# Kernel optimization log

Measured on AMD Instinct MI355X. Metric: run time of the kernel, lower is better.

Reference implementation:

```python
import jax, jax.numpy as jnp
import numpy as np

D_MODEL = 1024
N_LAYER = 8
VOCAB = 32000
D_INNER = 2048
D_STATE = 16
DT_RANK = 64  # ceil(d_model/16)
KCONV = 4
SEQ = 2048


def causal_depthwise_conv(u, w):
    # u: [l, d_inner], w: [d_inner, 1, K]; causal padding (K-1, 0), groups=d_inner
    x = u.T[None]  # [1, d_inner, l]
    y = jax.lax.conv_general_dilated(
        x, w, window_strides=(1,), padding=[(KCONV - 1, 0)],
        dimension_numbers=("NCH", "OIH", "NCH"), feature_group_count=u.shape[1])
    return y[0].T  # [l, d_inner]


def selective_scan(u, dt, A, B, C, Dp):
    # u,dt: [l,d_in]; A: [d_in,n]; B,C: [l,n]; D: [d_in]; bilinear discretization
    dt_A = dt[:, :, None] * A[None, :, :]          # [l, d_in, n]
    dt_B = dt[:, :, None] * B[:, None, :]          # [l, d_in, n]
    denom = 1.0 - dt_A / 2
    dA = (1.0 + dt_A / 2) / denom
    dB = dt_B / denom

    def step(h, inp):
        ui, dAi, dBi, Ci = inp
        h = dAi * h + dBi * ui[:, None]            # [d_in, n]
        return h, h @ Ci                           # y_i: [d_in]

    h0 = jnp.zeros((u.shape[1], A.shape[1]), dtype=u.dtype)
    _, y = jax.lax.scan(step, h0, (u, dA, dB, C))
    return y + u * Dp


def mamba_layer(x, Wres, Win, Wconv, WB, WC, Wdt1, Wdt2, bdt, logA, Dp, Wout):
    # RMS pre-norm (no learned scale)
    xn = x * jax.lax.rsqrt(jnp.mean(x * x, axis=-1, keepdims=True) + 1e-6)
    res = xn @ Wres.T                              # [l, d_inner]
    u = xn @ Win.T                                 # [l, d_inner]
    u = causal_depthwise_conv(u, Wconv)
    u = jax.nn.silu(u)
    A = -jnp.exp(logA)                             # [d_inner, n]
    B = u @ WB.T                                   # [l, n]
    C = u @ WC.T                                   # [l, n]
    dt = jax.nn.softplus((u @ Wdt1.T) @ Wdt2.T + bdt)
    y = selective_scan(u, dt, A, B, C, Dp)
    y = y * jax.nn.silu(res)
    return x + y @ Wout.T                          # residual


def setup_inputs() -> dict:
    key = jax.random.key(0)
    ks = jax.random.split(key, 12)
    L = N_LAYER
    token_ids = jax.random.randint(ks[0], (SEQ,), 0, VOCAB)
    embed = jax.random.normal(ks[1], (VOCAB, D_MODEL), jnp.float32) * 0.02
    Wres = jax.random.normal(ks[2], (L, D_INNER, D_MODEL), jnp.float32) * 0.02
    Win = jax.random.normal(ks[3], (L, D_INNER, D_MODEL), jnp.float32) * 0.02
    Wconv = jax.random.normal(ks[4], (L, D_INNER, 1, KCONV), jnp.float32) * 0.3
    WB = jax.random.normal(ks[5], (L, D_STATE, D_INNER), jnp.float32) * 0.02
    WC = jax.random.normal(ks[6], (L, D_STATE, D_INNER), jnp.float32) * 0.02
    Wdt1 = jax.random.normal(ks[7], (L, DT_RANK, D_INNER), jnp.float32) / np.sqrt(D_INNER)
    Wdt2 = jax.random.uniform(ks[8], (L, D_INNER, DT_RANK), jnp.float32,
                              minval=-1 / np.sqrt(DT_RANK), maxval=1 / np.sqrt(DT_RANK))
    # inverse-softplus of dt ~ U[1e-3, 1e-1] in log space
    dt0 = jnp.exp(jax.random.uniform(ks[9], (L, D_INNER)) * (np.log(0.1) - np.log(0.001)) + np.log(0.001))
    bdt = dt0 + jnp.log(-jnp.expm1(-dt0))
    logA = jnp.log(jnp.broadcast_to(jnp.arange(1, D_STATE + 1, dtype=jnp.float32),
                                    (L, D_INNER, D_STATE)))
    Dp = jnp.ones((L, D_INNER), jnp.float32)
    Wout = jax.random.normal(ks[10], (L, D_MODEL, D_INNER), jnp.float32) * 0.02
    return dict(token_ids=token_ids, embed=embed, Wres=Wres, Win=Win, Wconv=Wconv,
                WB=WB, WC=WC, Wdt1=Wdt1, Wdt2=Wdt2, bdt=bdt, logA=logA, Dp=Dp, Wout=Wout)


def reference(token_ids, embed, Wres, Win, Wconv, WB, WC, Wdt1, Wdt2, bdt, logA, Dp, Wout):
    x = embed[token_ids]  # [l, d_model]
    for i in range(Wres.shape[0]):
        x = mamba_layer(x, Wres[i], Win[i], Wconv[i], WB[i], WC[i],
                        Wdt1[i], Wdt2[i], bdt[i], logA[i], Dp[i], Wout[i])
    return x @ embed.T  # [l, vocab] logits (tied embedding)
```

## Files before the change

### kernel.cpp

```cpp
#include <hip/hip_runtime.h>

#define SEQ 2048
#define DMODEL 1024
#define DINNER 2048
#define DSTATE 16
#define DTRANK 64
#define NLAYER 8
#define VOCAB 32000
#define NCHUNK 32
#define CLEN 64
#define PZ 16

typedef float f32x4 __attribute__((ext_vector_type(4)));
typedef short bf16x8 __attribute__((ext_vector_type(8)));

__device__ __forceinline__ ushort f2bf(float f) {
  union { float f; unsigned u; } v; v.f = f;
  unsigned r = v.u + 0x7fffu + ((v.u >> 16) & 1u);
  return (ushort)(r >> 16);
}
__device__ __forceinline__ float bf2f(ushort b) {
  union { unsigned u; float f; } v; v.u = ((unsigned)b) << 16;
  return v.f;
}

__device__ __forceinline__ void lds_load16(const void* g, void* l) {
  __builtin_amdgcn_global_load_lds(
      (const __attribute__((address_space(1))) void*)g,
      (__attribute__((address_space(3))) void*)l, 16, 0, 0);
}

template<int BM, bool NTS>
__global__ __launch_bounds__(512, 2) void gemm8p_bt_bf16(
    const ushort* __restrict__ A, const ushort* __restrict__ B,
    float* __restrict__ C, int N, int K)
{
  constexpr int MFR = BM / 32;
  constexpr int MPP = MFR / 4;
  constexpr int ALOADS = BM / 128;
  __shared__ __align__(16) ushort As[2 * BM * 64];
  __shared__ __align__(16) ushort Bs[2 * 256 * 64];
  const int tid = threadIdx.x;
  const int lane = tid & 63;
  const int wid = tid >> 6;
  const int wr = wid >> 2, wc = wid & 3;
  const int rr = lane & 15, kq = lane >> 4;

  unsigned nwg = gridDim.x * gridDim.y;
  unsigned lb = blockIdx.y * gridDim.x + blockIdx.x;
  if ((nwg & 7u) == 0u) { unsigned cpx = nwg >> 3; lb = (lb & 7u) * cpx + (lb >> 3); }
  const int bm = (int)(lb % gridDim.x) * BM;
  const int bn = (int)(lb / gridDim.x) * 256;

  const ushort* Abase = A + (size_t)bm * K;
  const ushort* Bbase = B + (size_t)bn * K;

  auto stageA = [&](int buf, int h, int kt) {
    constexpr int HR = BM / 2;
#pragma unroll
    for (int L = 0; L < ALOADS; ++L) {
      int f = L * 512 + tid;
      int rl = f >> 3, g = f & 7;
      int gg = g ^ (rl & 7);
      lds_load16(Abase + (size_t)(h * HR + rl) * K + kt * 64 + gg * 8,
                 (void*)(As + buf * (BM * 64) + (h * HR + rl) * 64 + g * 8));
    }
  };
  auto stageB = [&](int buf, int h, int kt) {
#pragma unroll
    for (int L = 0; L < 2; ++L) {
      int f = L * 512 + tid;
      int rl = f >> 3, g = f & 7;
      int gg = g ^ (rl & 7);
      lds_load16(Bbase + (size_t)(h * 128 + rl) * K + kt * 64 + gg * 8,
                 (void*)(Bs + buf * (256 * 64) + (h * 128 + rl) * 64 + g * 8));
    }
  };
  auto rdA = [&](int buf, int r, int kbyte) {
    int sw = kbyte ^ ((r & 7) << 4);
    return *(const bf16x8*)(As + buf * (BM * 64) + r * 64 + (sw >> 1));
  };
  auto rdB = [&](int buf, int r, int kbyte) {
    int sw = kbyte ^ ((r & 7) << 4);
    return *(const bf16x8*)(Bs + buf * (256 * 64) + r * 64 + (sw >> 1));
  };

  f32x4 acc[MFR][4];
#pragma unroll
  for (int m = 0; m < MFR; ++m)
#pragma unroll
    for (int n = 0; n < 4; ++n) acc[m][n] = (f32x4){0.f, 0.f, 0.f, 0.f};

  const int NT = K >> 6;
  stageA(0, 0, 0); stageA(0, 1, 0); stageB(0, 0, 0); stageB(0, 1, 0);

  for (int t = 0; t < NT; ++t) {
    const int cur = t & 1;
    const bool more = (t + 1 < NT);
    if (more) stageA(cur ^ 1, 0, t + 1);
    if (more) {
      if constexpr (BM == 256) asm volatile("s_waitcnt vmcnt(2)" ::: "memory");
      else                     asm volatile("s_waitcnt vmcnt(1)" ::: "memory");
    } else {
      asm volatile("s_waitcnt vmcnt(0)" ::: "memory");
    }
    __syncthreads();

    bf16x8 bfr[4][2];
#pragma unroll
    for (int n = 0; n < 4; ++n)
#pragma unroll
      for (int kk = 0; kk < 2; ++kk)
        bfr[n][kk] = rdB(cur, wc * 64 + n * 16 + rr, kk * 64 + kq * 16);

#pragma unroll
    for (int mq = 0; mq < 4; ++mq) {
      if (mq == 1 && more) stageA(cur ^ 1, 1, t + 1);
      if (mq == 2 && more) stageB(cur ^ 1, 0, t + 1);
      if (mq == 3 && more) stageB(cur ^ 1, 1, t + 1);
      bf16x8 af[MPP][2];
#pragma unroll
      for (int mf = 0; mf < MPP; ++mf)
#pragma unroll
        for (int kk = 0; kk < 2; ++kk)
          af[mf][kk] = rdA(cur, wr * (BM / 2) + (mq * MPP + mf) * 16 + rr, kk * 64 + kq * 16);
      __builtin_amdgcn_s_setprio(1);
#pragma unroll
      for (int kk = 0; kk < 2; ++kk)
#pragma unroll
        for (int mf = 0; mf < MPP; ++mf)
#pragma unroll
          for (int n = 0; n < 4; ++n)
            acc[mq * MPP + mf][n] = __builtin_amdgcn_mfma_f32_16x16x32_bf16(
                af[mf][kk], bfr[n][kk], acc[mq * MPP + mf][n], 0, 0, 0);
      __builtin_amdgcn_s_setprio(0);
    }
    __syncthreads();
  }

  float* ep = (float*)Bs + wid * (16 * 68);
  const int cg = bn + wc * 64;
#pragma unroll
  for (int m = 0; m < MFR; ++m) {
    const int r0g = bm + wr * (BM / 2) + m * 16;
#pragma unroll
    for (int n = 0; n < 4; ++n)
#pragma unroll
      for (int j = 0; j < 4; ++j)
        ep[(kq * 4 + j) * 68 + n * 16 + rr] = acc[m][n][j];
#pragma unroll
    for (int i = 0; i < 4; ++i) {
      int row = i * 4 + kq;
      f32x4 v = *(const f32x4*)&ep[row * 68 + rr * 4];
      f32x4* dst = (f32x4*)&C[(size_t)(r0g + row) * N + cg + rr * 4];
      if constexpr (NTS) __builtin_nontemporal_store(v, dst);
      else *dst = v;
    }
  }
}

template<bool OUTBF>
__global__ __launch_bounds__(256, 2) void gemm2p_bt_bf16(
    const ushort* __restrict__ A, const ushort* __restrict__ B,
    void* __restrict__ Cv, int N, int K)
{
  __shared__ __align__(16) ushort As[2 * 128 * 64];
  __shared__ __align__(16) ushort Bs[2 * 128 * 64];
  const int tid = threadIdx.x;
  const int lane = tid & 63;
  const int wave = tid >> 6;
  const int wr = wave >> 1, wc = wave & 1;
  const int rr = lane & 15, kq = lane >> 4;

  unsigned nwg = gridDim.x * gridDim.y;
  unsigned lb = blockIdx.y * gridDim.x + blockIdx.x;
  if ((nwg & 7u) == 0u) { unsigned cpx = nwg >> 3; lb = (lb & 7u) * cpx + (lb >> 3); }
  const int bm = (int)(lb % gridDim.x) * 128;
  const int bn = (int)(lb / gridDim.x) * 128;

  const ushort* Abase = A + (size_t)bm * K;
  const ushort* Bbase = B + (size_t)bn * K;

  auto stage = [&](int buf, int kt) {
#pragma unroll
    for (int i = 0; i < 4; ++i) {
      int f = i * 256 + tid;
      int rl = f >> 3, g = f & 7;
      int gg = g ^ (rl & 7);
      lds_load16(Abase + (size_t)rl * K + kt * 64 + gg * 8,
                 (void*)(As + buf * 8192 + rl * 64 + g * 8));
      lds_load16(Bbase + (size_t)rl * K + kt * 64 + gg * 8,
                 (void*)(Bs + buf * 8192 + rl * 64 + g * 8));
    }
  };
  auto rdA = [&](int buf, int r, int kbyte) {
    int sw = kbyte ^ ((r & 7) << 4);
    return *(const bf16x8*)(As + buf * 8192 + r * 64 + (sw >> 1));
  };
  auto rdB = [&](int buf, int r, int kbyte) {
    int sw = kbyte ^ ((r & 7) << 4);
    return *(const bf16x8*)(Bs + buf * 8192 + r * 64 + (sw >> 1));
  };

  f32x4 acc[4][4];
#pragma unroll
  for (int m = 0; m < 4; ++m)
#pragma unroll
    for (int n = 0; n < 4; ++n) acc[m][n] = (f32x4){0.f, 0.f, 0.f, 0.f};

  const int NT = K >> 6;
  stage(0, 0);

  for (int t = 0; t < NT; ++t) {
    const int cur = t & 1;
    if (t + 1 < NT) {
      stage(cur ^ 1, t + 1);
      asm volatile("s_waitcnt vmcnt(8)" ::: "memory");
    } else {
      asm volatile("s_waitcnt vmcnt(0)" ::: "memory");
    }
    __syncthreads();
#pragma unroll
    for (int ks = 0; ks < 2; ++ks) {
      const int kbyte = ks * 64 + kq * 16;
      bf16x8 af[4], bfr[4];
#pragma unroll
      for (int m = 0; m < 4; ++m)
        af[m] = rdA(cur, wr * 64 + m * 16 + rr, kbyte);
#pragma unroll
      for (int n = 0; n < 4; ++n)
        bfr[n] = rdB(cur, wc * 64 + n * 16 + rr, kbyte);
      __builtin_amdgcn_s_setprio(1);
#pragma unroll
      for (int m = 0; m < 4; ++m)
#pragma unroll
        for (int n = 0; n < 4; ++n)
          acc[m][n] = __builtin_amdgcn_mfma_f32_16x16x32_bf16(af[m], bfr[n], acc[m][n], 0, 0, 0);
      __builtin_amdgcn_s_setprio(0);
    }
    __syncthreads();
  }

  float* ep = (float*)Bs + wave * (16 * 68);
  const int cg = bn + wc * 64;
#pragma unroll
  for (int m = 0; m < 4; ++m) {
    const int r0g = bm + wr * 64 + m * 16;
#pragma unroll
    for (int n = 0; n < 4; ++n)
#pragma unroll
      for (int j = 0; j < 4; ++j)
        ep[(kq * 4 + j) * 68 + n * 16 + rr] = acc[m][n][j];
#pragma unroll
    for (int i = 0; i < 4; ++i) {
      int row = i * 4 + kq;
      f32x4 v = *(const f32x4*)&ep[row * 68 + rr * 4];
      if constexpr (OUTBF) {
        ushort* C = (ushort*)Cv;
        ushort4 o = {f2bf(v.x), f2bf(v.y), f2bf(v.z), f2bf(v.w)};
        *(ushort4*)&C[(size_t)(r0g + row) * N + cg + rr * 4] = o;
      } else {
        float* C = (float*)Cv;
        *(f32x4*)&C[(size_t)(r0g + row) * N + cg + rr * 4] = v;
      }
    }
  }
}

__global__ __launch_bounds__(256) void gemm_btk_bf16(
    const ushort* __restrict__ A, const ushort* __restrict__ B,
    ushort* __restrict__ Cp, int M, int N, int K)
{
  __shared__ __align__(16) ushort As[128 * 64];
  __shared__ __align__(16) ushort Bs[128 * 64];
  const int tid = threadIdx.x;
  const int lane = tid & 63;
  const int wave = tid >> 6;
  const int wr = wave >> 1, wc = wave & 1;
  const int KC = K / gridDim.z;
  const int k0 = blockIdx.z * KC;

  unsigned nwg = gridDim.x * gridDim.y;
  unsigned lb = blockIdx.y * gridDim.x + blockIdx.x;
  if ((nwg & 7u) == 0u) {
    unsigned cpx = nwg >> 3;
    lb = (lb & 7u) * cpx + (lb >> 3);
  }
  const int bm = (lb % gridDim.x) * 128;
  const int bn = (lb / gridDim.x) * 128;
  const int rr = lane & 15, kq = lane >> 4;

  auto rdA = [&](int r, int kbyte) {
    int sw = kbyte ^ ((r & 7) << 4);
    return *(const bf16x8*)(As + r * 64 + (sw >> 1));
  };
  auto rdB = [&](int r, int kbyte) {
    int sw = kbyte ^ ((r & 7) << 4);
    return *(const bf16x8*)(Bs + r * 64 + (sw >> 1));
  };

  f32x4 acc[4][4];
#pragma unroll
  for (int m = 0; m < 4; ++m)
#pragma unroll
    for (int n = 0; n < 4; ++n) acc[m][n] = (f32x4){0.f, 0.f, 0.f, 0.f};

  for (int kt = 0; kt < KC; kt += 64) {
#pragma unroll
    for (int i = 0; i < 4; ++i) {
      int fb = i * 256 + tid;
      int row = fb >> 3, g = fb & 7;
      int gg = g ^ (row & 7);
      lds_load16(A + (size_t)(bm + row) * K + k0 + kt + gg * 8, (void*)(As + (size_t)fb * 8));
      lds_load16(B + (size_t)(bn + row) * K + k0 + kt + gg * 8, (void*)(Bs + (size_t)fb * 8));
    }
    asm volatile("s_waitcnt vmcnt(0)" ::: "memory");
    __syncthreads();
#pragma unroll
    for (int ks = 0; ks < 2; ++ks) {
      const int kbyte = ks * 64 + kq * 16;
      bf16x8 af[4], bfr[4];
#pragma unroll
      for (int m = 0; m < 4; ++m)
        af[m] = rdA(wr * 64 + m * 16 + rr, kbyte);
#pragma unroll
      for (int n = 0; n < 4; ++n)
        bfr[n] = rdB(wc * 64 + n * 16 + rr, kbyte);
#pragma unroll
      for (int m = 0; m < 4; ++m)
#pragma unroll
        for (int n = 0; n < 4; ++n)
          acc[m][n] = __builtin_amdgcn_mfma_f32_16x16x32_bf16(af[m], bfr[n], acc[m][n], 0, 0, 0);
    }
    __syncthreads();
  }
  ushort* C = Cp + (size_t)blockIdx.z * M * N;
#pragma unroll
  for (int m = 0; m < 4; ++m) {
    const int r0 = bm + wr * 64 + m * 16 + kq * 4;
#pragma unroll
    for (int n = 0; n < 4; ++n) {
      const int cc = bn + wc * 64 + n * 16 + rr;
#pragma unroll
      for (int j = 0; j < 4; ++j)
        C[(size_t)(r0 + j) * N + cc] = f2bf(acc[m][n][j]);
    }
  }
}

__global__ __launch_bounds__(256) void convproj_mfma(
    const ushort* __restrict__ resu0, const ushort* __restrict__ W,
    const float* __restrict__ Wconv, ushort* __restrict__ u,
    float* __restrict__ Cp, int M)
{
  __shared__ __align__(16) ushort u0s[131][128];
  __shared__ __align__(16) ushort As[2][128 * 64];
  __shared__ __align__(16) ushort Bs[2][128 * 64];
  const int tid = threadIdx.x;
  const int lane = tid & 63;
  const int wave = tid >> 6;
  const int wr = wave >> 1, wc = wave & 1;
  const int rr = lane & 15, kq = lane >> 4;
  const int bm = blockIdx.x * 128;
  const int kc = blockIdx.z * 128;

#pragma unroll
  for (int h = 0; h < 2; ++h)
#pragma unroll
    for (int i = 0; i < 4; ++i) {
      int f = i * 256 + tid;
      int rl = f >> 3, g = f & 7;
      int gg = g ^ (rl & 7);
      lds_load16(W + (size_t)rl * DINNER + kc + h * 64 + gg * 8,
                 (void*)(&Bs[h][rl * 64 + g * 8]));
    }

  for (int i = tid; i < 131 * 32; i += 256) {
    int row = i >> 5, c4 = (i & 31) * 4;
    int gr = bm - 3 + row;
    ushort4 v = {0, 0, 0, 0};
    if (gr >= 0)
      v = *(const ushort4*)&resu0[(size_t)gr * (2 * DINNER) + DINNER + kc + c4];
    *(ushort4*)&u0s[row][c4] = v;
  }
  __syncthreads();

  {
    const int c0 = (tid & 31) * 4;
    const int r0 = (tid >> 5) * 16;
    float4 w0 = *(const float4*)&Wconv[(kc + c0 + 0) * 4];
    float4 w1 = *(const float4*)&Wconv[(kc + c0 + 1) * 4];
    float4 w2 = *(const float4*)&Wconv[(kc + c0 + 2) * 4];
    float4 w3 = *(const float4*)&Wconv[(kc + c0 + 3) * 4];
    const int ks = c0 >> 6;
    const int cl = c0 & 63;
    for (int r = r0; r < r0 + 16; ++r) {
      ushort4 a0 = *(const ushort4*)&u0s[r + 0][c0];
      ushort4 a1 = *(const ushort4*)&u0s[r + 1][c0];
      ushort4 a2 = *(const ushort4*)&u0s[r + 2][c0];
      ushort4 a3 = *(const ushort4*)&u0s[r + 3][c0];
      float o0 = bf2f(a0.x) * w0.x + bf2f(a1.x) * w0.y + bf2f(a2.x) * w0.z + bf2f(a3.x) * w0.w;
      float o1 = bf2f(a0.y) * w1.x + bf2f(a1.y) * w1.y + bf2f(a2.y) * w1.z + bf2f(a3.y) * w1.w;
      float o2 = bf2f(a0.z) * w2.x + bf2f(a1.z) * w2.y + bf2f(a2.z) * w2.z + bf2f(a3.z) * w2.w;
      float o3 = bf2f(a0.w) * w3.x + bf2f(a1.w) * w3.y + bf2f(a2.w) * w3.z + bf2f(a3.w) * w3.w;
      o0 = o0 / (1.f + expf(-o0));
      o1 = o1 / (1.f + expf(-o1));
      o2 = o2 / (1.f + expf(-o2));
      o3 = o3 / (1.f + expf(-o3));
      ushort4 o = {f2bf(o0), f2bf(o1), f2bf(o2), f2bf(o3)};
      int sg = ((cl >> 3) ^ (r & 7)) * 8 + (cl & 7);
      *(ushort4*)&As[ks][r * 64 + sg] = o;
      *(ushort4*)&u[(size_t)(bm + r) * DINNER + kc + c0] = o;
    }
  }
  asm volatile("s_waitcnt vmcnt(0)" ::: "memory");
  __syncthreads();

  f32x4 acc[4][4];
#pragma unroll
  for (int m = 0; m < 4; ++m)
#pragma unroll
    for (int n = 0; n < 4; ++n) acc[m][n] = (f32x4){0.f, 0.f, 0.f, 0.f};

#pragma unroll
  for (int ks = 0; ks < 2; ++ks) {
#pragma unroll
    for (int kk = 0; kk < 2; ++kk) {
      const int kbyte = kk * 64 + kq * 16;
      bf16x8 af[4], bfr[4];
#pragma unroll
      for (int m = 0; m < 4; ++m) {
        int r = wr * 64 + m * 16 + rr;
        int sw = kbyte ^ ((r & 7) << 4);
        af[m] = *(const bf16x8*)&As[ks][r * 64 + (sw >> 1)];
      }
#pragma unroll
      for (int n = 0; n < 4; ++n) {
        int r = wc * 64 + n * 16 + rr;
        int sw = kbyte ^ ((r & 7) << 4);
        bfr[n] = *(const bf16x8*)&Bs[ks][r * 64 + (sw >> 1)];
      }
      __builtin_amdgcn_s_setprio(1);
#pragma unroll
      for (int m = 0; m < 4; ++m)
#pragma unroll
        for (int n = 0; n < 4; ++n)
          acc[m][n] = __builtin_amdgcn_mfma_f32_16x16x32_bf16(af[m], bfr[n], acc[m][n], 0, 0, 0);
      __builtin_amdgcn_s_setprio(0);
    }
  }

  float* C = Cp + (size_t)blockIdx.z * M * 128;
#pragma unroll
  for (int m = 0; m < 4; ++m) {
    const int r0 = bm + wr * 64 + m * 16 + kq * 4;
#pragma unroll
    for (int n = 0; n < 4; ++n) {
      const int cc = wc * 64 + n * 16 + rr;
#pragma unroll
      for (int j = 0; j < 4; ++j)
        C[(size_t)(r0 + j) * 128 + cc] = acc[m][n][j];
    }
  }
}

__global__ __launch_bounds__(256) void gemm_dt_bf16(
    const ushort* __restrict__ A, const ushort* __restrict__ W,
    const float* __restrict__ bias, ushort* __restrict__ dt)
{
  __shared__ __align__(16) ushort As[128 * 64];
  __shared__ __align__(16) ushort Bs[128 * 64];
  __shared__ float eps[4 * 16 * 68];
  const int tid = threadIdx.x;
  const int lane = tid & 63;
  const int wave = tid >> 6;
  const int wr = wave >> 1, wc = wave & 1;
  const int rr = lane & 15, kq = lane >> 4;
  const int bm = blockIdx.x * 128;
  const int bn = blockIdx.y * 128;

#pragma unroll
  for (int i = 0; i < 4; ++i) {
    int f = i * 256 + tid;
    int rl = f >> 3, g = f & 7;
    int gg = g ^ (rl & 7);
    lds_load16(A + (size_t)(bm + rl) * DTRANK + gg * 8, (void*)(As + (size_t)f * 8));
    lds_load16(W + (size_t)(bn + rl) * DTRANK + gg * 8, (void*)(Bs + (size_t)f * 8));
  }
  asm volatile("s_waitcnt vmcnt(0)" ::: "memory");
  __syncthreads();

  f32x4 acc[4][4];
#pragma unroll
  for (int m = 0; m < 4; ++m)
#pragma unroll
    for (int n = 0; n < 4; ++n) acc[m][n] = (f32x4){0.f, 0.f, 0.f, 0.f};

#pragma unroll
  for (int ks = 0; ks < 2; ++ks) {
    const int kbyte = ks * 64 + kq * 16;
    bf16x8 af[4], bfr[4];
#pragma unroll
    for (int m = 0; m < 4; ++m) {
      int r = wr * 64 + m * 16 + rr;
      int sw = kbyte ^ ((r & 7) << 4);
      af[m] = *(const bf16x8*)&As[r * 64 + (sw >> 1)];
    }
#pragma unroll
    for (int n = 0; n < 4; ++n) {
      int r = wc * 64 + n * 16 + rr;
      int sw = kbyte ^ ((r & 7) << 4);
      bfr[n] = *(const bf16x8*)&Bs[r * 64 + (sw >> 1)];
    }
#pragma unroll
    for (int m = 0; m < 4; ++m)
#pragma unroll
      for (int n = 0; n < 4; ++n)
        acc[m][n] = __builtin_amdgcn_mfma_f32_16x16x32_bf16(af[m], bfr[n], acc[m][n], 0, 0, 0);
  }
  __syncthreads();

  float* ep = eps + wave * (16 * 68);
  const int cgb = bn + wc * 64 + rr * 4;
  float4 b4 = *(const float4*)&bias[cgb];
#pragma unroll
  for (int m = 0; m < 4; ++m) {
    const int r0g = bm + wr * 64 + m * 16;
#pragma unroll
    for (int n = 0; n < 4; ++n)
#pragma unroll
      for (int j = 0; j < 4; ++j)
        ep[(kq * 4 + j) * 68 + n * 16 + rr] = acc[m][n][j];
#pragma unroll
    for (int i = 0; i < 4; ++i) {
      int row = i * 4 + kq;
      f32x4 v = *(const f32x4*)&ep[row * 68 + rr * 4];
      float v0 = v.x + b4.x, v1 = v.y + b4.y, v2 = v.z + b4.z, v3 = v.w + b4.w;
      v0 = (v0 > 20.f) ? v0 : log1pf(expf(v0));
      v1 = (v1 > 20.f) ? v1 : log1pf(expf(v1));
      v2 = (v2 > 20.f) ? v2 : log1pf(expf(v2));
      v3 = (v3 > 20.f) ? v3 : log1pf(expf(v3));
      ushort4 o = {f2bf(v0), f2bf(v1), f2bf(v2), f2bf(v3)};
      *(ushort4*)&dt[(size_t)(r0g + row) * DINNER + cgb] = o;
    }
  }
}

__global__ __launch_bounds__(256) void add3_rms_kernel(
    const ushort* __restrict__ P0, const ushort* __restrict__ P1,
    float* __restrict__ x, ushort* __restrict__ dst, int donorm)
{
  size_t o = (size_t)blockIdx.x * (DMODEL / 4) + threadIdx.x;
  ushort4 a = ((const ushort4*)P0)[o];
  ushort4 b = ((const ushort4*)P1)[o];
  float4 c = ((float4*)x)[o];
  c.x += bf2f(a.x) + bf2f(b.x);
  c.y += bf2f(a.y) + bf2f(b.y);
  c.z += bf2f(a.z) + bf2f(b.z);
  c.w += bf2f(a.w) + bf2f(b.w);
  ((float4*)x)[o] = c;
  float sc = 1.f;
  if (donorm) {
    float s = c.x * c.x + c.y * c.y + c.z * c.z + c.w * c.w;
#pragma unroll
    for (int off = 32; off > 0; off >>= 1) s += __shfl_down(s, off);
    __shared__ float ws[4];
    if ((threadIdx.x & 63) == 0) ws[threadIdx.x >> 6] = s;
    __syncthreads();
    float tot = ws[0] + ws[1] + ws[2] + ws[3];
    sc = rsqrtf(tot * (1.0f / DMODEL) + 1e-6f);
  }
  ushort4 o4 = {f2bf(c.x * sc), f2bf(c.y * sc), f2bf(c.z * sc), f2bf(c.w * sc)};
  ((ushort4*)dst)[o] = o4;
}

__global__ __launch_bounds__(256) void gather_rms_kernel(
    const int* __restrict__ ids, const float* __restrict__ embed,
    float* __restrict__ x, ushort* __restrict__ xnb)
{
  int row = blockIdx.x;
  int id = ids[row];
  float4 v = ((const float4*)(embed + (size_t)id * DMODEL))[threadIdx.x];
  size_t o = (size_t)row * (DMODEL / 4) + threadIdx.x;
  ((float4*)x)[o] = v;
  float s = v.x * v.x + v.y * v.y + v.z * v.z + v.w * v.w;
#pragma unroll
  for (int off = 32; off > 0; off >>= 1) s += __shfl_down(s, off);
  __shared__ float ws[4];
  if ((threadIdx.x & 63) == 0) ws[threadIdx.x >> 6] = s;
  __syncthreads();
  float tot = ws[0] + ws[1] + ws[2] + ws[3];
  float sc = rsqrtf(tot * (1.0f / DMODEL) + 1e-6f);
  ushort4 o4 = {f2bf(v.x * sc), f2bf(v.y * sc), f2bf(v.z * sc), f2bf(v.w * sc)};
  ((ushort4*)xnb)[o] = o4;
}

__global__ __launch_bounds__(256) void proj_reduce(
    const float* __restrict__ Cp, float* __restrict__ bcdt,
    ushort* __restrict__ dtinb, int M)
{
  int idx = blockIdx.x * 256 + threadIdx.x;
  int row = idx / 96, col = idx - row * 96;
  float s = 0.f;
#pragma unroll
  for (int c = 0; c < PZ; ++c) s += Cp[(size_t)c * M * 128 + (size_t)row * 128 + col];
  if (col < 32) bcdt[(size_t)row * 96 + col] = s;
  else dtinb[(size_t)row * 64 + (col - 32)] = f2bf(s);
}

__global__ __launch_bounds__(256) void scan_pass1(
    const ushort* __restrict__ dt, const ushort* __restrict__ u,
    const float* __restrict__ bcdt, const float* __restrict__ logA,
    float* __restrict__ P, float* __restrict__ S)
{
  const int tid = threadIdx.x;
  const int n = tid & 15, dl = tid >> 4;
  const int dbase = blockIdx.x * 16;
  const int c = blockIdx.y;
  const int t0 = c * CLEN;
  const int d = dbase + dl;
  const float Aval = -expf(logA[d * DSTATE + n]);
  __shared__ float sdt[CLEN][16], su[CLEN][16], sB[CLEN][16];
  {
    int tt = tid >> 2, j0 = (tid & 3) * 4;
    ushort4 rd = *(const ushort4*)&dt[(size_t)(t0 + tt) * DINNER + dbase + j0];
    ushort4 ru = *(const ushort4*)&u[(size_t)(t0 + tt) * DINNER + dbase + j0];
    sdt[tt][j0 + 0] = bf2f(rd.x); sdt[tt][j0 + 1] = bf2f(rd.y);
    sdt[tt][j0 + 2] = bf2f(rd.z); sdt[tt][j0 + 3] = bf2f(rd.w);
    su[tt][j0 + 0] = bf2f(ru.x); su[tt][j0 + 1] = bf2f(ru.y);
    su[tt][j0 + 2] = bf2f(ru.z); su[tt][j0 + 3] = bf2f(ru.w);
    *(float4*)&sB[tt][j0] = *(const float4*)&bcdt[(size_t)(t0 + tt) * 96 + j0];
  }
  __syncthreads();
  float h = 0.f, pr = 1.f;
#pragma unroll 8
  for (int i = 0; i < CLEN; ++i) {
    float dtv = sdt[i][dl], uv = su[i][dl], Bv = sB[i][n];
    float dtA = dtv * Aval;
    float rinv = __builtin_amdgcn_rcpf(1.f - 0.5f * dtA);
    float dA = (1.f + 0.5f * dtA) * rinv;
    float dBu = dtv * Bv * rinv * uv;
    h = dA * h + dBu;
    pr *= dA;
  }
  size_t idx = (size_t)c * (DINNER * DSTATE) + (size_t)d * DSTATE + n;
  P[idx] = pr;
  S[idx] = h;
}

__global__ __launch_bounds__(256) void scan_pass2(
    const ushort* __restrict__ dt, const ushort* __restrict__ u,
    const float* __restrict__ bcdt, const float* __restrict__ logA,
    const float* __restrict__ Dp, const float* __restrict__ P,
    const float* __restrict__ S, const ushort* __restrict__ resu0,
    ushort* __restrict__ y2b)
{
  const int tid = threadIdx.x;
  const int n = tid & 15, dl = tid >> 4;
  const int dbase = blockIdx.x * 16;
  const int c = blockIdx.y;
  const int t0 = c * CLEN;
  const int d = dbase + dl;
  const float Aval = -expf(logA[d * DSTATE + n]);
  const float Dpv = Dp[d];
  __shared__ float sdt[CLEN][16], su[CLEN][16], sB[CLEN][16], sC[CLEN][16], sres[CLEN][16];
  {
    int tt = tid >> 2, j0 = (tid & 3) * 4;
    ushort4 rd = *(const ushort4*)&dt[(size_t)(t0 + tt) * DINNER + dbase + j0];
    ushort4 ru = *(const ushort4*)&u[(size_t)(t0 + tt) * DINNER + dbase + j0];
    ushort4 rr4 = *(const ushort4*)&resu0[(size_t)(t0 + tt) * (2 * DINNER) + dbase + j0];
    sdt[tt][j0 + 0] = bf2f(rd.x); sdt[tt][j0 + 1] = bf2f(rd.y);
    sdt[tt][j0 + 2] = bf2f(rd.z); sdt[tt][j0 + 3] = bf2f(rd.w);
    su[tt][j0 + 0] = bf2f(ru.x); su[tt][j0 + 1] = bf2f(ru.y);
    su[tt][j0 + 2] = bf2f(ru.z); su[tt][j0 + 3] = bf2f(ru.w);
    sres[tt][j0 + 0] = bf2f(rr4.x); sres[tt][j0 + 1] = bf2f(rr4.y);
    sres[tt][j0 + 2] = bf2f(rr4.z); sres[tt][j0 + 3] = bf2f(rr4.w);
    *(float4*)&sB[tt][j0] = *(const float4*)&bcdt[(size_t)(t0 + tt) * 96 + j0];
    *(float4*)&sC[tt][j0] = *(const float4*)&bcdt[(size_t)(t0 + tt) * 96 + 16 + j0];
  }
  float h = 0.f;
  {
    const size_t base = (size_t)d * DSTATE + n;
#pragma unroll 4
    for (int cc = 0; cc < c; ++cc) {
      size_t o = (size_t)cc * (DINNER * DSTATE) + base;
      h = P[o] * h + S[o];
    }
  }
  __syncthreads();
#pragma unroll 4
  for (int i = 0; i < CLEN; ++i) {
    float dtv = sdt[i][dl], uv = su[i][dl];
    float dtA = dtv * Aval;
    float rinv = __builtin_amdgcn_rcpf(1.f - 0.5f * dtA);
    float dA = (1.f + 0.5f * dtA) * rinv;
    float dBu = dtv * sB[i][n] * rinv * uv;
    h = dA * h + dBu;
    float p = h * sC[i][n];
    p += __shfl_xor(p, 1);
    p += __shfl_xor(p, 2);
    p += __shfl_xor(p, 4);
    p += __shfl_xor(p, 8);
    if (n == 0) {
      float rv = sres[i][dl];
      float yv = (p + uv * Dpv) * (rv / (1.f + expf(-rv)));
      y2b[(size_t)(t0 + i) * DINNER + d] = f2bf(yv);
    }
  }
}

__global__ __launch_bounds__(256) void preproc_kernel(
    const float* __restrict__ embed, const float* __restrict__ Wres,
    const float* __restrict__ Win, const float* __restrict__ Wout,
    const float* __restrict__ WB, const float* __restrict__ WC,
    const float* __restrict__ Wdt1, const float* __restrict__ Wdt2,
    ushort* __restrict__ eb, ushort* __restrict__ wcatb,
    ushort* __restrict__ woutb, ushort* __restrict__ wbcdtb,
    ushort* __restrict__ wdt2b)
{
  const size_t S0 = (size_t)VOCAB * DMODEL / 4;
  const size_t S1 = (size_t)NLAYER * 2 * DINNER * DMODEL / 4;
  const size_t S2 = (size_t)NLAYER * DMODEL * DINNER / 4;
  const size_t S3 = (size_t)NLAYER * 128 * DINNER / 4;
  const size_t S4 = (size_t)NLAYER * DINNER * DTRANK / 4;
  size_t i4 = (size_t)blockIdx.x * 256 + threadIdx.x;
  float4 v;
  ushort* dst;
  size_t di;
  if (i4 < S0) {
    v = ((const float4*)embed)[i4];
    dst = eb; di = i4;
  } else if (i4 < S0 + S1) {
    size_t j4 = i4 - S0;
    size_t e0 = j4 * 4;
    int k = (int)(e0 & (DMODEL - 1));
    int r = (int)((e0 >> 10) & (2 * DINNER - 1));
    int l = (int)(e0 >> 22);
    const float* src = (r < DINNER)
        ? &Wres[(((size_t)l * DINNER + r) << 10) + k]
        : &Win[(((size_t)l * DINNER + (r - DINNER)) << 10) + k];
    v = *(const float4*)src;
    dst = wcatb; di = j4;
  } else if (i4 < S0 + S1 + S2) {
    size_t j4 = i4 - S0 - S1;
    v = ((const float4*)Wout)[j4];
    dst = woutb; di = j4;
  } else if (i4 < S0 + S1 + S2 + S3) {
    size_t j4 = i4 - S0 - S1 - S2;
    int k4 = (int)(j4 & (DINNER / 4 - 1));
    int row = (int)((j4 >> 9) & 127);
    int l = (int)(j4 >> 16);
    int k = k4 * 4;
    v = (float4){0.f, 0.f, 0.f, 0.f};
    if (row < 16)       v = *(const float4*)&WB[((size_t)l * DSTATE + row) * DINNER + k];
    else if (row < 32)  v = *(const float4*)&WC[((size_t)l * DSTATE + (row - 16)) * DINNER + k];
    else if (row < 96)  v = *(const float4*)&Wdt1[((size_t)l * DTRANK + (row - 32)) * DINNER + k];
    dst = wbcdtb; di = j4;
  } else if (i4 < S0 + S1 + S2 + S3 + S4) {
    size_t j4 = i4 - S0 - S1 - S2 - S3;
    v = ((const float4*)Wdt2)[j4];
    dst = wdt2b; di = j4;
  } else {
    return;
  }
  ushort4 o = {f2bf(v.x), f2bf(v.y), f2bf(v.z), f2bf(v.w)};
  ((ushort4*)dst)[di] = o;
}

extern "C" void kernel_launch(void* const* d_in, const int* in_sizes, int n_in,
                              void* d_out, int out_size, void* d_ws, size_t ws_size,
                              hipStream_t stream) {
  (void)in_sizes; (void)n_in; (void)out_size;
  const int* token_ids = (const int*)d_in[0];
  const float* embed = (const float*)d_in[1];
  const float* Wres = (const float*)d_in[2];
  const float* Win = (const float*)d_in[3];
  const float* Wconv = (const float*)d_in[4];
  const float* WB = (const float*)d_in[5];
  const float* WC = (const float*)d_in[6];
  const float* Wdt1 = (const float*)d_in[7];
  const float* Wdt2 = (const float*)d_in[8];
  const float* bdt = (const float*)d_in[9];
  const float* logA = (const float*)d_in[10];
  const float* Dp = (const float*)d_in[11];
  const float* Wout = (const float*)d_in[12];
  float* out = (float*)d_out;

  char* w = (char*)d_ws;
  auto alloc = [&](size_t bytes) {
    char* p = w;
    w += (bytes + 255) & ~(size_t)255;
    return p;
  };
  ushort* eb     = (ushort*)alloc((size_t)VOCAB * DMODEL * 2);
  ushort* wcatb  = (ushort*)alloc((size_t)NLAYER * 2 * DINNER * DMODEL * 2);
  ushort* woutb  = (ushort*)alloc((size_t)NLAYER * DMODEL * DINNER * 2);
  ushort* wbcdtb = (ushort*)alloc((size_t)NLAYER * 128 * DINNER * 2);
  ushort* wdt2b  = (ushort*)alloc((size_t)NLAYER * DINNER * DTRANK * 2);
  float* x       = (float*)alloc((size_t)SEQ * DMODEL * 4);
  ushort* xnb    = (ushort*)alloc((size_t)SEQ * DMODEL * 2);
  ushort* resu0  = (ushort*)alloc((size_t)SEQ * 2 * DINNER * 2);
  ushort* u      = (ushort*)alloc((size_t)SEQ * DINNER * 2);
  float* bcdt    = (float*)alloc((size_t)SEQ * 96 * 4);
  ushort* dtinb  = (ushort*)alloc((size_t)SEQ * 64 * 2);
  ushort* dt     = (ushort*)alloc((size_t)SEQ * DINNER * 2);
  float* Cp      = (float*)alloc((size_t)PZ * SEQ * 128 * 4);
  ushort* Cp2    = (ushort*)alloc((size_t)2 * SEQ * DMODEL * 2);
  float* Pbuf    = (float*)alloc((size_t)NCHUNK * DINNER * DSTATE * 4);
  float* Sbuf    = (float*)alloc((size_t)NCHUNK * DINNER * DSTATE * 4);
  ushort* y2b    = (ushort*)alloc((size_t)SEQ * DINNER * 2);
  ushort* xb     = (ushort*)alloc((size_t)SEQ * DMODEL * 2);
  if ((size_t)(w - (char*)d_ws) > ws_size) return;

  {
    size_t total4 = (size_t)VOCAB * DMODEL / 4
                  + (size_t)NLAYER * 2 * DINNER * DMODEL / 4
                  + (size_t)NLAYER * DMODEL * DINNER / 4
                  + (size_t)NLAYER * 128 * DINNER / 4
                  + (size_t)NLAYER * DINNER * DTRANK / 4;
    int nblk = (int)((total4 + 255) / 256);
    preproc_kernel<<<nblk, 256, 0, stream>>>(
        embed, Wres, Win, Wout, WB, WC, Wdt1, Wdt2,
        eb, wcatb, woutb, wbcdtb, wdt2b);
  }
  gather_rms_kernel<<<SEQ, 256, 0, stream>>>(token_ids, embed, x, xnb);

  for (int i = 0; i < NLAYER; ++i) {
    const ushort* wcati = wcatb + (size_t)i * 2 * DINNER * DMODEL;
    const ushort* wouti = woutb + (size_t)i * DMODEL * DINNER;
    const float* wconvi = Wconv + (size_t)i * DINNER * 4;
    const ushort* wbcdtbi = wbcdtb + (size_t)i * 128 * DINNER;
    const ushort* wdt2bi = wdt2b + (size_t)i * DINNER * DTRANK;
    const float* bdti = bdt + (size_t)i * DINNER;
    const float* logAi = logA + (size_t)i * DINNER * DSTATE;
    const float* Dpi = Dp + (size_t)i * DINNER;

    gemm2p_bt_bf16<true><<<dim3(SEQ / 128, 2 * DINNER / 128), 256, 0, stream>>>(
        xnb, wcati, resu0, 2 * DINNER, DMODEL);
    convproj_mfma<<<dim3(SEQ / 128, 1, PZ), 256, 0, stream>>>(
        resu0, wbcdtbi, wconvi, u, Cp, SEQ);
    proj_reduce<<<SEQ * 96 / 256, 256, 0, stream>>>(Cp, bcdt, dtinb, SEQ);
    gemm_dt_bf16<<<dim3(SEQ / 128, DINNER / 128), 256, 0, stream>>>(
        dtinb, wdt2bi, bdti, dt);
    dim3 gs(DINNER / 16, NCHUNK);
    scan_pass1<<<gs, 256, 0, stream>>>(dt, u, bcdt, logAi, Pbuf, Sbuf);
    scan_pass2<<<gs, 256, 0, stream>>>(dt, u, bcdt, logAi, Dpi, Pbuf, Sbuf, resu0, y2b);
    gemm_btk_bf16<<<dim3(SEQ / 128, DMODEL / 128, 2), 256, 0, stream>>>(
        y2b, wouti, Cp2, SEQ, DMODEL, DINNER);
    add3_rms_kernel<<<SEQ, 256, 0, stream>>>(
        Cp2, Cp2 + (size_t)SEQ * DMODEL, x,
        (i < NLAYER - 1) ? xnb : xb, (i < NLAYER - 1) ? 1 : 0);
  }
  gemm8p_bt_bf16<256, true><<<dim3(SEQ / 256, VOCAB / 256), 512, 0, stream>>>(
      xb, eb, out, VOCAB, DMODEL);
}
```

Baseline: 1.910 ms.

## Fuse dt projection GEMM and softplus into both scan passes

Measured after the change: 1.986 ms. +4.0%, slower.

```diff
diff --git a/kernel.cpp b/kernel.cpp
--- a/kernel.cpp
+++ b/kernel.cpp
@@ -464,88 +464,6 @@
   }
 }
 
-__global__ __launch_bounds__(256) void gemm_dt_bf16(
-    const ushort* __restrict__ A, const ushort* __restrict__ W,
-    const float* __restrict__ bias, ushort* __restrict__ dt)
-{
-  __shared__ __align__(16) ushort As[128 * 64];
-  __shared__ __align__(16) ushort Bs[128 * 64];
-  __shared__ float eps[4 * 16 * 68];
-  const int tid = threadIdx.x;
-  const int lane = tid & 63;
-  const int wave = tid >> 6;
-  const int wr = wave >> 1, wc = wave & 1;
-  const int rr = lane & 15, kq = lane >> 4;
-  const int bm = blockIdx.x * 128;
-  const int bn = blockIdx.y * 128;
-
-#pragma unroll
-  for (int i = 0; i < 4; ++i) {
-    int f = i * 256 + tid;
-    int rl = f >> 3, g = f & 7;
-    int gg = g ^ (rl & 7);
-    lds_load16(A + (size_t)(bm + rl) * DTRANK + gg * 8, (void*)(As + (size_t)f * 8));
-    lds_load16(W + (size_t)(bn + rl) * DTRANK + gg * 8, (void*)(Bs + (size_t)f * 8));
-  }
-  asm volatile("s_waitcnt vmcnt(0)" ::: "memory");
-  __syncthreads();
-
-  f32x4 acc[4][4];
-#pragma unroll
-  for (int m = 0; m < 4; ++m)
-#pragma unroll
-    for (int n = 0; n < 4; ++n) acc[m][n] = (f32x4){0.f, 0.f, 0.f, 0.f};
-
-#pragma unroll
-  for (int ks = 0; ks < 2; ++ks) {
-    const int kbyte = ks * 64 + kq * 16;
-    bf16x8 af[4], bfr[4];
-#pragma unroll
-    for (int m = 0; m < 4; ++m) {
-      int r = wr * 64 + m * 16 + rr;
-      int sw = kbyte ^ ((r & 7) << 4);
-      af[m] = *(const bf16x8*)&As[r * 64 + (sw >> 1)];
-    }
-#pragma unroll
-    for (int n = 0; n < 4; ++n) {
-      int r = wc * 64 + n * 16 + rr;
-      int sw = kbyte ^ ((r & 7) << 4);
-      bfr[n] = *(const bf16x8*)&Bs[r * 64 + (sw >> 1)];
-    }
-#pragma unroll
-    for (int m = 0; m < 4; ++m)
-#pragma unroll
-      for (int n = 0; n < 4; ++n)
-        acc[m][n] = __builtin_amdgcn_mfma_f32_16x16x32_bf16(af[m], bfr[n], acc[m][n], 0, 0, 0);
-  }
-  __syncthreads();
-
-  float* ep = eps + wave * (16 * 68);
-  const int cgb = bn + wc * 64 + rr * 4;
-  float4 b4 = *(const float4*)&bias[cgb];
-#pragma unroll
-  for (int m = 0; m < 4; ++m) {
-    const int r0g = bm + wr * 64 + m * 16;
-#pragma unroll
-    for (int n = 0; n < 4; ++n)
-#pragma unroll
-      for (int j = 0; j < 4; ++j)
-        ep[(kq * 4 + j) * 68 + n * 16 + rr] = acc[m][n][j];
-#pragma unroll
-    for (int i = 0; i < 4; ++i) {
-      int row = i * 4 + kq;
-      f32x4 v = *(const f32x4*)&ep[row * 68 + rr * 4];
-      float v0 = v.x + b4.x, v1 = v.y + b4.y, v2 = v.z + b4.z, v3 = v.w + b4.w;
-      v0 = (v0 > 20.f) ? v0 : log1pf(expf(v0));
-      v1 = (v1 > 20.f) ? v1 : log1pf(expf(v1));
-      v2 = (v2 > 20.f) ? v2 : log1pf(expf(v2));
-      v3 = (v3 > 20.f) ? v3 : log1pf(expf(v3));
-      ushort4 o = {f2bf(v0), f2bf(v1), f2bf(v2), f2bf(v3)};
-      *(ushort4*)&dt[(size_t)(r0g + row) * DINNER + cgb] = o;
-    }
-  }
-}
-
 __global__ __launch_bounds__(256) void add3_rms_kernel(
     const ushort* __restrict__ P0, const ushort* __restrict__ P1,
     float* __restrict__ x, ushort* __restrict__ dst, int donorm)
@@ -608,9 +526,35 @@
   else dtinb[(size_t)row * 64 + (col - 32)] = f2bf(s);
 }
 
+__device__ __forceinline__ void compute_dt_tile(
+    const ushort* sDtin , const ushort* sW2 ,
+    const float* __restrict__ bdt, int dbase,
+    float sdt[CLEN][16], int tid)
+{
+  const int wave = tid >> 6;
+  const int lane = tid & 63;
+  f32x4 dacc = (f32x4){0.f, 0.f, 0.f, 0.f};
+#pragma unroll
+  for (int ks = 0; ks < 2; ++ks) {
+    bf16x8 af = *(const bf16x8*)&sDtin[(wave * 16 + (lane & 15)) * 64 + ks * 32 + (lane >> 4) * 8];
+    bf16x8 bf = *(const bf16x8*)&sW2[(lane & 15) * 64 + ks * 32 + (lane >> 4) * 8];
+    dacc = __builtin_amdgcn_mfma_f32_16x16x32_bf16(af, bf, dacc, 0, 0, 0);
+  }
+  const int col = lane & 15;
+  const float bv = bdt[dbase + col];
+#pragma unroll
+  for (int j = 0; j < 4; ++j) {
+    int trow = wave * 16 + (lane >> 4) * 4 + j;
+    float v = dacc[j] + bv;
+    v = (v > 20.f) ? v : log1pf(expf(v));
+    sdt[trow][col] = v;
+  }
+}
+
 __global__ __launch_bounds__(256) void scan_pass1(
-    const ushort* __restrict__ dt, const ushort* __restrict__ u,
-    const float* __restrict__ bcdt, const float* __restrict__ logA,
+    const ushort* __restrict__ dtinb, const ushort* __restrict__ u,
+    const float* __restrict__ bcdt, const ushort* __restrict__ wdt2,
+    const float* __restrict__ bdt, const float* __restrict__ logA,
     float* __restrict__ P, float* __restrict__ S)
 {
   const int tid = threadIdx.x;
@@ -621,16 +565,25 @@
   const int d = dbase + dl;
   const float Aval = -expf(logA[d * DSTATE + n]);
   __shared__ float sdt[CLEN][16], su[CLEN][16], sB[CLEN][16];
+  __shared__ __align__(16) ushort sDtin[64 * 64];
+  __shared__ __align__(16) ushort sW2[16 * 64];
   {
     int tt = tid >> 2, j0 = (tid & 3) * 4;
-    ushort4 rd = *(const ushort4*)&dt[(size_t)(t0 + tt) * DINNER + dbase + j0];
     ushort4 ru = *(const ushort4*)&u[(size_t)(t0 + tt) * DINNER + dbase + j0];
-    sdt[tt][j0 + 0] = bf2f(rd.x); sdt[tt][j0 + 1] = bf2f(rd.y);
-    sdt[tt][j0 + 2] = bf2f(rd.z); sdt[tt][j0 + 3] = bf2f(rd.w);
     su[tt][j0 + 0] = bf2f(ru.x); su[tt][j0 + 1] = bf2f(ru.y);
     su[tt][j0 + 2] = bf2f(ru.z); su[tt][j0 + 3] = bf2f(ru.w);
     *(float4*)&sB[tt][j0] = *(const float4*)&bcdt[(size_t)(t0 + tt) * 96 + j0];
   }
+  for (int i = tid; i < 64 * 16; i += 256) {
+    int row = i >> 4, c4 = (i & 15) * 4;
+    *(ushort4*)&sDtin[row * 64 + c4] = *(const ushort4*)&dtinb[(size_t)(t0 + row) * 64 + c4];
+  }
+  if (tid < 16 * 16) {
+    int row = tid >> 4, c4 = (tid & 15) * 4;
+    *(ushort4*)&sW2[row * 64 + c4] = *(const ushort4*)&wdt2[(size_t)(dbase + row) * DTRANK + c4];
+  }
+  __syncthreads();
+  compute_dt_tile(sDtin, sW2, bdt, dbase, sdt, tid);
   __syncthreads();
   float h = 0.f, pr = 1.f;
 #pragma unroll 8
@@ -649,8 +602,9 @@
 }
 
 __global__ __launch_bounds__(256) void scan_pass2(
-    const ushort* __restrict__ dt, const ushort* __restrict__ u,
-    const float* __restrict__ bcdt, const float* __restrict__ logA,
+    const ushort* __restrict__ dtinb, const ushort* __restrict__ u,
+    const float* __restrict__ bcdt, const ushort* __restrict__ wdt2,
+    const float* __restrict__ bdt, const float* __restrict__ logA,
     const float* __restrict__ Dp, const float* __restrict__ P,
     const float* __restrict__ S, const ushort* __restrict__ resu0,
     ushort* __restrict__ y2b)
@@ -664,19 +618,26 @@
   const float Aval = -expf(logA[d * DSTATE + n]);
   const float Dpv = Dp[d];
   __shared__ float sdt[CLEN][16], su[CLEN][16], sB[CLEN][16], sC[CLEN][16], sres[CLEN][16];
+  __shared__ __align__(16) ushort sDtin[64 * 64];
+  __shared__ __align__(16) ushort sW2[16 * 64];
   {
     int tt = tid >> 2, j0 = (tid & 3) * 4;
-    ushort4 rd = *(const ushort4*)&dt[(size_t)(t0 + tt) * DINNER + dbase + j0];
     ushort4 ru = *(const ushort4*)&u[(size_t)(t0 + tt) * DINNER + dbase + j0];
     ushort4 rr4 = *(const ushort4*)&resu0[(size_t)(t0 + tt) * (2 * DINNER) + dbase + j0];
-    sdt[tt][j0 + 0] = bf2f(rd.x); sdt[tt][j0 + 1] = bf2f(rd.y);
-    sdt[tt][j0 + 2] = bf2f(rd.z); sdt[tt][j0 + 3] = bf2f(rd.w);
     su[tt][j0 + 0] = bf2f(ru.x); su[tt][j0 + 1] = bf2f(ru.y);
     su[tt][j0 + 2] = bf2f(ru.z); su[tt][j0 + 3] = bf2f(ru.w);
     sres[tt][j0 + 0] = bf2f(rr4.x); sres[tt][j0 + 1] = bf2f(rr4.y);
     sres[tt][j0 + 2] = bf2f(rr4.z); sres[tt][j0 + 3] = bf2f(rr4.w);
     *(float4*)&sB[tt][j0] = *(const float4*)&bcdt[(size_t)(t0 + tt) * 96 + j0];
     *(float4*)&sC[tt][j0] = *(const float4*)&bcdt[(size_t)(t0 + tt) * 96 + 16 + j0];
+  }
+  for (int i = tid; i < 64 * 16; i += 256) {
+    int row = i >> 4, c4 = (i & 15) * 4;
+    *(ushort4*)&sDtin[row * 64 + c4] = *(const ushort4*)&dtinb[(size_t)(t0 + row) * 64 + c4];
+  }
+  if (tid < 16 * 16) {
+    int row = tid >> 4, c4 = (tid & 15) * 4;
+    *(ushort4*)&sW2[row * 64 + c4] = *(const ushort4*)&wdt2[(size_t)(dbase + row) * DTRANK + c4];
   }
   float h = 0.f;
   {
@@ -687,6 +648,8 @@
       h = P[o] * h + S[o];
     }
   }
+  __syncthreads();
+  compute_dt_tile(sDtin, sW2, bdt, dbase, sdt, tid);
   __syncthreads();
 #pragma unroll 4
   for (int i = 0; i < CLEN; ++i) {
@@ -803,7 +766,6 @@
   ushort* u      = (ushort*)alloc((size_t)SEQ * DINNER * 2);
   float* bcdt    = (float*)alloc((size_t)SEQ * 96 * 4);
   ushort* dtinb  = (ushort*)alloc((size_t)SEQ * 64 * 2);
-  ushort* dt     = (ushort*)alloc((size_t)SEQ * DINNER * 2);
   float* Cp      = (float*)alloc((size_t)PZ * SEQ * 128 * 4);
   ushort* Cp2    = (ushort*)alloc((size_t)2 * SEQ * DMODEL * 2);
   float* Pbuf    = (float*)alloc((size_t)NCHUNK * DINNER * DSTATE * 4);
@@ -840,11 +802,10 @@
     convproj_mfma<<<dim3(SEQ / 128, 1, PZ), 256, 0, stream>>>(
         resu0, wbcdtbi, wconvi, u, Cp, SEQ);
     proj_reduce<<<SEQ * 96 / 256, 256, 0, stream>>>(Cp, bcdt, dtinb, SEQ);
-    gemm_dt_bf16<<<dim3(SEQ / 128, DINNER / 128), 256, 0, stream>>>(
-        dtinb, wdt2bi, bdti, dt);
     dim3 gs(DINNER / 16, NCHUNK);
-    scan_pass1<<<gs, 256, 0, stream>>>(dt, u, bcdt, logAi, Pbuf, Sbuf);
-    scan_pass2<<<gs, 256, 0, stream>>>(dt, u, bcdt, logAi, Dpi, Pbuf, Sbuf, resu0, y2b);
+    scan_pass1<<<gs, 256, 0, stream>>>(dtinb, u, bcdt, wdt2bi, bdti, logAi, Pbuf, Sbuf);
+    scan_pass2<<<gs, 256, 0, stream>>>(dtinb, u, bcdt, wdt2bi, bdti, logAi, Dpi,
+                                       Pbuf, Sbuf, resu0, y2b);
     gemm_btk_bf16<<<dim3(SEQ / 128, DMODEL / 128, 2), 256, 0, stream>>>(
         y2b, wouti, Cp2, SEQ, DMODEL, DINNER);
     add3_rms_kernel<<<SEQ, 256, 0, stream>>>(
```
